# Kernel tuning notes

Hardware: AMD Instinct MI355X
Metric: run time of the kernel (lower is better)

The kernel has to match this reference:

```python
import jax, jax.numpy as jnp
import numpy as np

B = 262144   # n_batch
DT = 0.01    # filter period T_filter from reset_state


def _quat_mul(q, r):
    # Hamilton product, q,r: [B,4] in (w,x,y,z)
    w1, x1, y1, z1 = q[:, 0], q[:, 1], q[:, 2], q[:, 3]
    w2, x2, y2, z2 = r[:, 0], r[:, 1], r[:, 2], r[:, 3]
    return jnp.stack([
        w1 * w2 - x1 * x2 - y1 * y2 - z1 * z2,
        w1 * x2 + x1 * w2 + y1 * z2 - z1 * y2,
        w1 * y2 - x1 * z2 + y1 * w2 + z1 * x2,
        w1 * z2 + x1 * y2 - y1 * x2 + z1 * w2,
    ], axis=-1)


def _inject(state, err):
    # state: [B,7,1] = [p(3); q(4)], err: [B,6,1] = [dp(3); dtheta(3)]
    p = state[:, :3, 0] + err[:, :3, 0]
    q = state[:, 3:, 0]
    dth = 0.5 * err[:, 3:, 0]
    dq = jnp.concatenate([jnp.ones_like(dth[:, :1]), dth], axis=-1)  # small-angle quat
    qn = _quat_mul(q, dq)
    qn = qn / jnp.linalg.norm(qn, axis=-1, keepdims=True)
    return jnp.concatenate([p, qn], axis=-1)[:, :, None]


def _Xdx(state):
    # ESKF Jacobian of nominal state wrt error state: [B,7,6]
    q = state[:, 3:, 0]
    bsz = q.shape[0]
    w, xq, y, z = q[:, 0], q[:, 1], q[:, 2], q[:, 3]
    Qd = 0.5 * jnp.stack([
        jnp.stack([-xq, -y, -z], -1),
        jnp.stack([w, -z, y], -1),
        jnp.stack([z, w, -xq], -1),
        jnp.stack([-y, xq, w], -1),
    ], axis=1)  # [B,4,3]
    I3 = jnp.broadcast_to(jnp.eye(3, dtype=state.dtype), (bsz, 3, 3))
    top = jnp.concatenate([I3, jnp.zeros((bsz, 3, 3), state.dtype)], axis=-1)
    bot = jnp.concatenate([jnp.zeros((bsz, 4, 3), state.dtype), Qd], axis=-1)
    return jnp.concatenate([top, bot], axis=1)


def setup_inputs() -> dict:
    key = jax.random.key(0)
    k1, k2, k3 = jax.random.split(key, 3)
    x = jax.random.normal(k1, (14, B), dtype=jnp.float32)
    p = jax.random.normal(k2, (B, 3), dtype=jnp.float32)
    q = jax.random.normal(k3, (B, 4), dtype=jnp.float32)
    q = q / jnp.linalg.norm(q, axis=-1, keepdims=True)
    state = jnp.concatenate([p, q], axis=-1)[:, :, None]  # [B,7,1]
    # covariances as in reset_state (diagonal, batched)
    covariance = jnp.tile(jnp.diag(jnp.array([1e-3] * 3 + [0.2] * 3, jnp.float32))[None], (B, 1, 1))
    Q = jnp.tile(jnp.diag(jnp.array([1e-4] * 3 + [2e-4] * 3, jnp.float32))[None], (B, 1, 1))
    R = jnp.tile(jnp.diag(jnp.array([1e-6] * 3 + [1e-4] * 4, jnp.float32))[None], (B, 1, 1))
    return {"x": x, "state": state, "covariance": covariance, "Q": Q, "R": R}


def reference(x, state, covariance, Q, R):
    # --- unpack forward args (mirrors forward(): permute(2,1,0)) ---
    twist = x[8:14].T[:, :, None]        # [B,6,1] control
    measurement = x[0:7].T[:, :, None]   # [B,7,1]
    # --- predict: F = I6, B_matrix = dt * I6 ---
    error_state_prior = DT * twist                       # B_matrix @ u
    predict_state = _inject(state, error_state_prior)    # [B,7,1]
    P = covariance + Q                                   # F P F^T + Q with F = I
    # --- update ---
    H = _Xdx(state)                                      # Hx = I7, so H = Xdx: [B,7,6]
    Ht = jnp.swapaxes(H, 1, 2)                           # [B,6,7]
    S = H @ P @ Ht + R                                   # [B,7,7]
    K = P @ Ht @ jnp.linalg.inv(S)                       # [B,6,7]
    innovation = measurement - predict_state             # [B,7,1]
    error_state = K @ innovation                         # [B,6,1]
    I6 = jnp.eye(6, dtype=P.dtype)
    P_new = (I6[None] - K @ H) @ P                       # stored as self.covariance (side effect)
    new_state = _inject(predict_state, error_state)      # [B,7,1]
    del P_new  # forward() returns only the state
    return new_state
```

## Files before the change

### kernel.cpp

```cpp
#include <hip/hip_runtime.h>

#define DT_C 0.01f

__device__ __forceinline__ void gload_lds16(const float* g, float* l) {
    __builtin_amdgcn_global_load_lds(
        (const __attribute__((address_space(1))) void*)g,
        (__attribute__((address_space(3))) void*)l,
        16, 0, 0);
}

__global__ __launch_bounds__(256, 2) void eskf_kernel(
    const float* __restrict__ x,
    const float* __restrict__ state,
    const float* __restrict__ cov,
    const float* __restrict__ Qm,
    const float* __restrict__ Rm,
    float* __restrict__ out,
    int B)
{
    __shared__ float ldsR[256 * 49];
    __shared__ float ldsS[256 * 7];

    const int tid  = threadIdx.x;
    const int lane = tid & 63;
    const int wave = tid >> 6;
    const int b    = blockIdx.x * 256 + tid;
    const int eb   = blockIdx.x * 256 + wave * 64;

    {
        const float* gs = state + (size_t)eb * 7;
        float*       ls = ldsS + wave * (64 * 7);
        gload_lds16(gs + 4 * lane, ls + 4 * lane);
        if (lane < 48) gload_lds16(gs + 4 * (64 + lane), ls + 4 * (64 + lane));

        const float* gr = Rm + (size_t)eb * 49;
        float*       lr = ldsR + wave * (64 * 49);
#pragma unroll
        for (int k = 0; k < 12; ++k)
            gload_lds16(gr + 4 * (k * 64 + lane), lr + 4 * (k * 64 + lane));
        if (lane < 16)
            gload_lds16(gr + 4 * (768 + lane), lr + 4 * (768 + lane));
    }

    float4 cv[9], qv[9];
    {
        const float4* c4 = (const float4*)(cov + (size_t)b * 36);
        const float4* q4 = (const float4*)(Qm  + (size_t)b * 36);
#pragma unroll
        for (int i = 0; i < 9; ++i) cv[i] = c4[i];
#pragma unroll
        for (int i = 0; i < 9; ++i) qv[i] = q4[i];
    }

    float meas[7], tw[6];
#pragma unroll
    for (int i = 0; i < 7; ++i) meas[i] = x[i * B + b];
#pragma unroll
    for (int i = 0; i < 6; ++i) tw[i] = x[(8 + i) * B + b];

    float P[36];
#pragma unroll
    for (int i = 0; i < 9; ++i) {
        P[4 * i + 0] = cv[i].x + qv[i].x;
        P[4 * i + 1] = cv[i].y + qv[i].y;
        P[4 * i + 2] = cv[i].z + qv[i].z;
        P[4 * i + 3] = cv[i].w + qv[i].w;
    }

    asm volatile("s_waitcnt vmcnt(0)" ::: "memory");

    float st[7];
    {
        const float* ls = ldsS + wave * (64 * 7) + lane * 7;
#pragma unroll
        for (int i = 0; i < 7; ++i) st[i] = ls[i];
    }

    float S[7][7];
    {
        const float* lr = ldsR + wave * (64 * 49) + lane * 49;
#pragma unroll
        for (int i = 0; i < 7; ++i)
#pragma unroll
            for (int j = 0; j < 7; ++j) S[i][j] = lr[i * 7 + j];
    }

    float ps[7];
    {
        float d0 = 0.5f * DT_C * tw[3], d1 = 0.5f * DT_C * tw[4], d2 = 0.5f * DT_C * tw[5];
        ps[0] = st[0] + DT_C * tw[0];
        ps[1] = st[1] + DT_C * tw[1];
        ps[2] = st[2] + DT_C * tw[2];
        float w = st[3], xx = st[4], yy = st[5], zz = st[6];
        float qw = w - xx * d0 - yy * d1 - zz * d2;
        float qx = w * d0 + xx + yy * d2 - zz * d1;
        float qy = w * d1 - xx * d2 + yy + zz * d0;
        float qz = w * d2 + xx * d1 - yy * d0 + zz;
        float inv = rsqrtf(qw * qw + qx * qx + qy * qy + qz * qz);
        ps[3] = qw * inv; ps[4] = qx * inv; ps[5] = qy * inv; ps[6] = qz * inv;
    }

    float Qd[4][3];
    {
        float w = st[3], xx = st[4], yy = st[5], zz = st[6];
        Qd[0][0] = -0.5f * xx; Qd[0][1] = -0.5f * yy; Qd[0][2] = -0.5f * zz;
        Qd[1][0] =  0.5f * w;  Qd[1][1] = -0.5f * zz; Qd[1][2] =  0.5f * yy;
        Qd[2][0] =  0.5f * zz; Qd[2][1] =  0.5f * w;  Qd[2][2] = -0.5f * xx;
        Qd[3][0] = -0.5f * yy; Qd[3][1] =  0.5f * xx; Qd[3][2] =  0.5f * w;
    }

#pragma unroll
    for (int i = 0; i < 3; ++i)
#pragma unroll
        for (int j = 0; j < 3; ++j)
            S[i][j] += P[i * 6 + j];

    float T[4][6];
#pragma unroll
    for (int i = 0; i < 4; ++i)
#pragma unroll
        for (int c = 0; c < 6; ++c) {
            float acc = 0.f;
#pragma unroll
            for (int k = 0; k < 3; ++k) acc += Qd[i][k] * P[(3 + k) * 6 + c];
            T[i][c] = acc;
        }

#pragma unroll
    for (int i = 0; i < 4; ++i)
#pragma unroll
        for (int j = 0; j < 3; ++j) S[3 + i][j] += T[i][j];

#pragma unroll
    for (int i = 0; i < 3; ++i)
#pragma unroll
        for (int j = 0; j < 4; ++j) {
            float acc = 0.f;
#pragma unroll
            for (int k = 0; k < 3; ++k) acc += P[i * 6 + 3 + k] * Qd[j][k];
            S[i][3 + j] += acc;
        }

#pragma unroll
    for (int i = 0; i < 4; ++i)
#pragma unroll
        for (int j = 0; j < 4; ++j) {
            float acc = 0.f;
#pragma unroll
            for (int l = 0; l < 3; ++l) acc += T[i][3 + l] * Qd[j][l];
            S[3 + i][3 + j] += acc;
        }

    float y[7];
#pragma unroll
    for (int i = 0; i < 7; ++i) y[i] = meas[i] - ps[i];

#pragma unroll
    for (int k = 0; k < 7; ++k) {
        float inv = 1.0f / S[k][k];
#pragma unroll
        for (int i = k + 1; i < 7; ++i) {
            float f = S[i][k] * inv;
#pragma unroll
            for (int j = k + 1; j < 7; ++j) S[i][j] -= f * S[k][j];
            y[i] -= f * y[k];
        }
    }
#pragma unroll
    for (int k = 6; k >= 0; --k) {
        float acc = y[k];
#pragma unroll
        for (int j = k + 1; j < 7; ++j) acc -= S[k][j] * y[j];
        y[k] = acc / S[k][k];
    }

    float z6[6];
    z6[0] = y[0]; z6[1] = y[1]; z6[2] = y[2];
#pragma unroll
    for (int c = 0; c < 3; ++c) {
        float acc = 0.f;
#pragma unroll
        for (int i = 0; i < 4; ++i) acc += Qd[i][c] * y[3 + i];
        z6[3 + c] = acc;
    }
    float es[6];
#pragma unroll
    for (int i = 0; i < 6; ++i) {
        float acc = 0.f;
#pragma unroll
        for (int j = 0; j < 6; ++j) acc += P[i * 6 + j] * z6[j];
        es[i] = acc;
    }

    float o0 = ps[0] + es[0];
    float o1 = ps[1] + es[1];
    float o2 = ps[2] + es[2];
    float d0 = 0.5f * es[3], d1 = 0.5f * es[4], d2 = 0.5f * es[5];
    float w = ps[3], xx = ps[4], yy = ps[5], zz = ps[6];
    float qw = w - xx * d0 - yy * d1 - zz * d2;
    float qx = w * d0 + xx + yy * d2 - zz * d1;
    float qy = w * d1 - xx * d2 + yy + zz * d0;
    float qz = w * d2 + xx * d1 - yy * d0 + zz;
    float inv = rsqrtf(qw * qw + qx * qx + qy * qy + qz * qz);

    {
        float* ol = ldsS + wave * (64 * 7) + lane * 7;
        ol[0] = o0; ol[1] = o1; ol[2] = o2;
        ol[3] = qw * inv; ol[4] = qx * inv; ol[5] = qy * inv; ol[6] = qz * inv;
        asm volatile("s_waitcnt lgkmcnt(0)" ::: "memory");

        float4*       og = (float4*)(out + (size_t)eb * 7);
        const float4* lf = (const float4*)(ldsS + wave * (64 * 7));
        og[lane] = lf[lane];
        if (lane < 48) og[64 + lane] = lf[64 + lane];
    }
}

extern "C" void kernel_launch(void* const* d_in, const int* in_sizes, int n_in,
                              void* d_out, int out_size, void* d_ws, size_t ws_size,
                              hipStream_t stream) {
    const float* x     = (const float*)d_in[0];
    const float* state = (const float*)d_in[1];
    const float* cov   = (const float*)d_in[2];
    const float* Qm    = (const float*)d_in[3];
    const float* Rm    = (const float*)d_in[4];
    float* out = (float*)d_out;
    int B = in_sizes[1] / 7;
    int grid = B / 256;
    eskf_kernel<<<grid, 256, 0, stream>>>(x, state, cov, Qm, Rm, out, B);
}
```

Before: 168.6 us.

## Stage covariance and Q through LDS with one-wave blocks

Switches to 64-thread blocks, with each wave owning its own LDS region. The per-thread strided float4 loads of covariance and Q are replaced by coalesced global_load_lds staging, and P is then read from LDS. The goal is better-coalesced global reads for the 36-float-per-element matrices and finer-grained scheduling. The cost is more LDS per wave (about 33 KB per 64 elements), which can limit occupancy, plus 36-float-stride LDS reads that may cause bank conflicts.

```diff
diff --git a/kernel.cpp b/kernel.cpp
--- a/kernel.cpp
+++ b/kernel.cpp
@@ -9,7 +9,7 @@
         16, 0, 0);
 }
 
-__global__ __launch_bounds__(256, 2) void eskf_kernel(
+__global__ __launch_bounds__(64, 2) void eskf_kernel(
     const float* __restrict__ x,
     const float* __restrict__ state,
     const float* __restrict__ cov,
@@ -18,38 +18,37 @@
     float* __restrict__ out,
     int B)
 {
-    __shared__ float ldsR[256 * 49];
-    __shared__ float ldsS[256 * 7];
-
-    const int tid  = threadIdx.x;
-    const int lane = tid & 63;
-    const int wave = tid >> 6;
-    const int b    = blockIdx.x * 256 + tid;
-    const int eb   = blockIdx.x * 256 + wave * 64;
-
-    {
+    __shared__ float ldsC[64 * 36];
+    __shared__ float ldsQ[64 * 36];
+    __shared__ float ldsR[64 * 49];
+    __shared__ float ldsS[64 * 7];
+
+    const int lane = threadIdx.x;
+    const int eb   = blockIdx.x * 64;
+    const int b    = eb + lane;
+
+    {
+        const float* gc = cov + (size_t)eb * 36;
+#pragma unroll
+        for (int k = 0; k < 9; ++k)
+            gload_lds16(gc + 4 * (k * 64 + lane), ldsC + 4 * (k * 64 + lane));
+
+        const float* gq = Qm + (size_t)eb * 36;
+#pragma unroll
+        for (int k = 0; k < 9; ++k)
+            gload_lds16(gq + 4 * (k * 64 + lane), ldsQ + 4 * (k * 64 + lane));
+
+        const float* gr = Rm + (size_t)eb * 49;
+#pragma unroll
+        for (int k = 0; k < 12; ++k)
+            gload_lds16(gr + 4 * (k * 64 + lane), ldsR + 4 * (k * 64 + lane));
+        if (lane < 16)
+            gload_lds16(gr + 4 * (768 + lane), ldsR + 4 * (768 + lane));
+
         const float* gs = state + (size_t)eb * 7;
-        float*       ls = ldsS + wave * (64 * 7);
-        gload_lds16(gs + 4 * lane, ls + 4 * lane);
-        if (lane < 48) gload_lds16(gs + 4 * (64 + lane), ls + 4 * (64 + lane));
-
-        const float* gr = Rm + (size_t)eb * 49;
-        float*       lr = ldsR + wave * (64 * 49);
-#pragma unroll
-        for (int k = 0; k < 12; ++k)
-            gload_lds16(gr + 4 * (k * 64 + lane), lr + 4 * (k * 64 + lane));
-        if (lane < 16)
-            gload_lds16(gr + 4 * (768 + lane), lr + 4 * (768 + lane));
-    }
-
-    float4 cv[9], qv[9];
-    {
-        const float4* c4 = (const float4*)(cov + (size_t)b * 36);
-        const float4* q4 = (const float4*)(Qm  + (size_t)b * 36);
-#pragma unroll
-        for (int i = 0; i < 9; ++i) cv[i] = c4[i];
-#pragma unroll
-        for (int i = 0; i < 9; ++i) qv[i] = q4[i];
+        gload_lds16(gs + 4 * lane, ldsS + 4 * lane);
+        if (lane < 48)
+            gload_lds16(gs + 4 * (64 + lane), ldsS + 4 * (64 + lane));
     }
 
     float meas[7], tw[6];
@@ -58,27 +57,32 @@
 #pragma unroll
     for (int i = 0; i < 6; ++i) tw[i] = x[(8 + i) * B + b];
 
+    asm volatile("s_waitcnt vmcnt(0)" ::: "memory");
+
     float P[36];
-#pragma unroll
-    for (int i = 0; i < 9; ++i) {
-        P[4 * i + 0] = cv[i].x + qv[i].x;
-        P[4 * i + 1] = cv[i].y + qv[i].y;
-        P[4 * i + 2] = cv[i].z + qv[i].z;
-        P[4 * i + 3] = cv[i].w + qv[i].w;
-    }
-
-    asm volatile("s_waitcnt vmcnt(0)" ::: "memory");
+    {
+        const float4* c4 = (const float4*)(ldsC + lane * 36);
+        const float4* q4 = (const float4*)(ldsQ + lane * 36);
+#pragma unroll
+        for (int i = 0; i < 9; ++i) {
+            float4 a = c4[i], bb = q4[i];
+            P[4 * i + 0] = a.x + bb.x;
+            P[4 * i + 1] = a.y + bb.y;
+            P[4 * i + 2] = a.z + bb.z;
+            P[4 * i + 3] = a.w + bb.w;
+        }
+    }
 
     float st[7];
     {
-        const float* ls = ldsS + wave * (64 * 7) + lane * 7;
+        const float* ls = ldsS + lane * 7;
 #pragma unroll
         for (int i = 0; i < 7; ++i) st[i] = ls[i];
     }
 
     float S[7][7];
     {
-        const float* lr = ldsR + wave * (64 * 49) + lane * 49;
+        const float* lr = ldsR + lane * 49;
 #pragma unroll
         for (int i = 0; i < 7; ++i)
 #pragma unroll
@@ -204,13 +208,13 @@
     float inv = rsqrtf(qw * qw + qx * qx + qy * qy + qz * qz);
 
     {
-        float* ol = ldsS + wave * (64 * 7) + lane * 7;
+        float* ol = ldsS + lane * 7;
         ol[0] = o0; ol[1] = o1; ol[2] = o2;
         ol[3] = qw * inv; ol[4] = qx * inv; ol[5] = qy * inv; ol[6] = qz * inv;
         asm volatile("s_waitcnt lgkmcnt(0)" ::: "memory");
 
         float4*       og = (float4*)(out + (size_t)eb * 7);
-        const float4* lf = (const float4*)(ldsS + wave * (64 * 7));
+        const float4* lf = (const float4*)ldsS;
         og[lane] = lf[lane];
         if (lane < 48) og[64 + lane] = lf[64 + lane];
     }
@@ -226,6 +230,6 @@
     const float* Rm    = (const float*)d_in[4];
     float* out = (float*)d_out;
     int B = in_sizes[1] / 7;
-    int grid = B / 256;
-    eskf_kernel<<<grid, 256, 0, stream>>>(x, state, cov, Qm, Rm, out, B);
+    int grid = B / 64;
+    eskf_kernel<<<grid, 64, 0, stream>>>(x, state, cov, Qm, Rm, out, B);
 }
```

New measurement: 167.7 us. Within noise of the previous version (-0.5%).
